# Optimization experiments

Hardware: AMD Instinct MI355X
Metric: run time of the kernel (lower is better)

The kernel has to match this reference:

```python
import jax, jax.numpy as jnp
import numpy as np

N_NODES = 131072
N_EDGES = 8388608
NUM_GRAPHS = 1024
GAMMA = 1.0


def setup_inputs() -> dict:
    key = jax.random.key(0)
    k1, k2, k3 = jax.random.split(key, 3)
    node_pos = jax.random.normal(k1, (N_NODES, 2), dtype=jnp.float32)
    full_edge_index = jax.random.randint(k2, (2, N_EDGES), 0, N_NODES, dtype=jnp.int64)
    batch_idx = jnp.sort(jax.random.randint(k3, (N_NODES,), 0, NUM_GRAPHS, dtype=jnp.int64))
    return {"node_pos": node_pos, "full_edge_index": full_edge_index, "batch_idx": batch_idx}


def reference(node_pos, full_edge_index, batch_idx):
    # gather edge endpoints: [E, 2] each
    start = node_pos[full_edge_index[0]]
    end = node_pos[full_edge_index[1]]
    # Euclidean length per edge, then exponential distance decay
    eu = jnp.linalg.norm(end - start, axis=1)          # [E]
    edge_occlusion = jnp.exp(-GAMMA * eu)              # [E]
    # scatter-sum per graph, keyed by graph id of the source node
    index = batch_idx[full_edge_index[0]]              # [E]
    graph_occlusion = jax.ops.segment_sum(edge_occlusion, index, num_segments=NUM_GRAPHS)
    # reduce = torch.mean over graphs
    return jnp.mean(graph_occlusion)
```

## Files before the change

### kernel.cpp

```cpp
#include <hip/hip_runtime.h>


#define N_EDGES_C   8388608
#define GRID1       2048
#define BLOCK1      256
#define TOTAL_THR   (GRID1 * BLOCK1)
#define N_GROUPS    (N_EDGES_C / 4)
#define GROUPS_PER_THREAD (N_GROUPS / TOTAL_THR)
#define INV_NUM_GRAPHS (1.0f / 1024.0f)

typedef int v4i __attribute__((ext_vector_type(4)));

__global__ __launch_bounds__(BLOCK1) void occlusion_partial(
    const float2* __restrict__ pos,
    const v4i*    __restrict__ src4,
    const v4i*    __restrict__ dst4,
    float*        __restrict__ partials)
{
    const int tid = blockIdx.x * blockDim.x + threadIdx.x;

    v4i s[GROUPS_PER_THREAD], d[GROUPS_PER_THREAD];
    #pragma unroll
    for (int j = 0; j < GROUPS_PER_THREAD; ++j) {
        s[j] = __builtin_nontemporal_load(&src4[tid + j * TOTAL_THR]);
        d[j] = __builtin_nontemporal_load(&dst4[tid + j * TOTAL_THR]);
    }

    float2 ps[16], pd[16];
    #pragma unroll
    for (int j = 0; j < GROUPS_PER_THREAD; ++j) {
        #pragma unroll
        for (int k = 0; k < 4; ++k) {
            ps[j * 4 + k] = pos[s[j][k]];
            pd[j * 4 + k] = pos[d[j][k]];
        }
    }

    float acc0 = 0.f, acc1 = 0.f, acc2 = 0.f, acc3 = 0.f;
    #pragma unroll
    for (int k = 0; k < 4; ++k) {
        float dx, dy;
        dx = pd[k +  0].x - ps[k +  0].x;  dy = pd[k +  0].y - ps[k +  0].y;
        acc0 += __expf(-sqrtf(dx * dx + dy * dy));
        dx = pd[k +  4].x - ps[k +  4].x;  dy = pd[k +  4].y - ps[k +  4].y;
        acc1 += __expf(-sqrtf(dx * dx + dy * dy));
        dx = pd[k +  8].x - ps[k +  8].x;  dy = pd[k +  8].y - ps[k +  8].y;
        acc2 += __expf(-sqrtf(dx * dx + dy * dy));
        dx = pd[k + 12].x - ps[k + 12].x;  dy = pd[k + 12].y - ps[k + 12].y;
        acc3 += __expf(-sqrtf(dx * dx + dy * dy));
    }
    float acc = (acc0 + acc1) + (acc2 + acc3);

    #pragma unroll
    for (int off = 32; off > 0; off >>= 1)
        acc += __shfl_down(acc, off, 64);

    __shared__ float wave_sums[BLOCK1 / 64];
    const int lane = threadIdx.x & 63;
    const int wid  = threadIdx.x >> 6;
    if (lane == 0) wave_sums[wid] = acc;
    __syncthreads();

    if (threadIdx.x == 0) {
        partials[blockIdx.x] = (wave_sums[0] + wave_sums[1]) +
                               (wave_sums[2] + wave_sums[3]);
    }
}

__global__ __launch_bounds__(256) void occlusion_final(
    const float* __restrict__ partials,
    float*       __restrict__ out)
{
    float a = 0.f;
    #pragma unroll
    for (int i = 0; i < GRID1 / 256; ++i)
        a += partials[threadIdx.x + i * 256];

    #pragma unroll
    for (int off = 32; off > 0; off >>= 1)
        a += __shfl_down(a, off, 64);

    __shared__ float w[4];
    if ((threadIdx.x & 63) == 0) w[threadIdx.x >> 6] = a;
    __syncthreads();
    if (threadIdx.x == 0)
        out[0] = ((w[0] + w[1]) + (w[2] + w[3])) * INV_NUM_GRAPHS;
}

extern "C" void kernel_launch(void* const* d_in, const int* in_sizes, int n_in,
                              void* d_out, int out_size, void* d_ws, size_t ws_size,
                              hipStream_t stream) {
    const float* node_pos = (const float*)d_in[0];
    const int*   edge_idx = (const int*)d_in[1];

    const int E = in_sizes[1] / 2;
    const int* src = edge_idx;
    const int* dst = edge_idx + E;

    float* partials = (float*)d_ws;
    float* out = (float*)d_out;

    occlusion_partial<<<GRID1, BLOCK1, 0, stream>>>(
        reinterpret_cast<const float2*>(node_pos),
        reinterpret_cast<const v4i*>(src),
        reinterpret_cast<const v4i*>(dst),
        partials);
    occlusion_final<<<1, 256, 0, stream>>>(partials, out);
}
```

Before: 166.8 us.

## Stage first quarter of node positions as half2 in LDS per block

Each 1024-thread block first copies the first 32768 node positions into shared memory, converted to half2, then loops over its edge groups. Endpoints with index below that bound are read from LDS and the rest from global memory. The grid shrinks to 256 blocks of 1024 threads and the final reduce changes to match. The aim is to replace about a quarter of the random global gathers with LDS reads. In exchange every block re-reads and converts the table, the 128KB of LDS limits occupancy, and positions lose precision to fp16.

Measured after the change: 166.5 us. Within noise of the previous version (-0.2%).

```diff
diff --git a/kernel.cpp b/kernel.cpp
--- a/kernel.cpp
+++ b/kernel.cpp
@@ -1,12 +1,14 @@
 #include <hip/hip_runtime.h>
+#include <hip/hip_fp16.h>
 
 
 #define N_EDGES_C   8388608
-#define GRID1       2048
-#define BLOCK1      256
+#define STAGED      32768
+#define BLOCK1      1024
+#define GRID1       256
 #define TOTAL_THR   (GRID1 * BLOCK1)
 #define N_GROUPS    (N_EDGES_C / 4)
-#define GROUPS_PER_THREAD (N_GROUPS / TOTAL_THR)
+#define GPT         (N_GROUPS / TOTAL_THR)
 #define INV_NUM_GRAPHS (1.0f / 1024.0f)
 
 typedef int v4i __attribute__((ext_vector_type(4)));
@@ -17,36 +19,55 @@
     const v4i*    __restrict__ dst4,
     float*        __restrict__ partials)
 {
-    const int tid = blockIdx.x * blockDim.x + threadIdx.x;
+    __shared__ __half2 tab[STAGED];
 
-    v4i s[GROUPS_PER_THREAD], d[GROUPS_PER_THREAD];
-    #pragma unroll
-    for (int j = 0; j < GROUPS_PER_THREAD; ++j) {
-        s[j] = __builtin_nontemporal_load(&src4[tid + j * TOTAL_THR]);
-        d[j] = __builtin_nontemporal_load(&dst4[tid + j * TOTAL_THR]);
-    }
-
-    float2 ps[16], pd[16];
-    #pragma unroll
-    for (int j = 0; j < GROUPS_PER_THREAD; ++j) {
+    {
+        const float4* p4 = reinterpret_cast<const float4*>(pos);
         #pragma unroll
-        for (int k = 0; k < 4; ++k) {
-            ps[j * 4 + k] = pos[s[j][k]];
-            pd[j * 4 + k] = pos[d[j][k]];
+        for (int i = threadIdx.x; i < STAGED / 2; i += BLOCK1) {
+            float4 v = p4[i];
+            tab[2 * i + 0] = __floats2half2_rn(v.x, v.y);
+            tab[2 * i + 1] = __floats2half2_rn(v.z, v.w);
         }
     }
+    __syncthreads();
+
+    const int tid = blockIdx.x * BLOCK1 + threadIdx.x;
 
     float acc0 = 0.f, acc1 = 0.f, acc2 = 0.f, acc3 = 0.f;
     #pragma unroll
-    for (int k = 0; k < 4; ++k) {
+    for (int j = 0; j < GPT; ++j) {
+        const int g = tid + j * TOTAL_THR;
+        const v4i s = __builtin_nontemporal_load(&src4[g]);
+        const v4i d = __builtin_nontemporal_load(&dst4[g]);
+
+        float2 ps[4], pd[4];
+        #pragma unroll
+        for (int k = 0; k < 4; ++k) {
+            const int is = s[k];
+            const int id = d[k];
+            if (is < STAGED) {
+                __half2 h = tab[is];
+                ps[k] = make_float2(__low2float(h), __high2float(h));
+            } else {
+                ps[k] = pos[is];
+            }
+            if (id < STAGED) {
+                __half2 h = tab[id];
+                pd[k] = make_float2(__low2float(h), __high2float(h));
+            } else {
+                pd[k] = pos[id];
+            }
+        }
+
         float dx, dy;
-        dx = pd[k +  0].x - ps[k +  0].x;  dy = pd[k +  0].y - ps[k +  0].y;
+        dx = pd[0].x - ps[0].x;  dy = pd[0].y - ps[0].y;
         acc0 += __expf(-sqrtf(dx * dx + dy * dy));
-        dx = pd[k +  4].x - ps[k +  4].x;  dy = pd[k +  4].y - ps[k +  4].y;
+        dx = pd[1].x - ps[1].x;  dy = pd[1].y - ps[1].y;
         acc1 += __expf(-sqrtf(dx * dx + dy * dy));
-        dx = pd[k +  8].x - ps[k +  8].x;  dy = pd[k +  8].y - ps[k +  8].y;
+        dx = pd[2].x - ps[2].x;  dy = pd[2].y - ps[2].y;
         acc2 += __expf(-sqrtf(dx * dx + dy * dy));
-        dx = pd[k + 12].x - ps[k + 12].x;  dy = pd[k + 12].y - ps[k + 12].y;
+        dx = pd[3].x - ps[3].x;  dy = pd[3].y - ps[3].y;
         acc3 += __expf(-sqrtf(dx * dx + dy * dy));
     }
     float acc = (acc0 + acc1) + (acc2 + acc3);
@@ -55,15 +76,18 @@
     for (int off = 32; off > 0; off >>= 1)
         acc += __shfl_down(acc, off, 64);
 
-    __shared__ float wave_sums[BLOCK1 / 64];
+    __syncthreads();
+    float* ws = reinterpret_cast<float*>(tab);
     const int lane = threadIdx.x & 63;
     const int wid  = threadIdx.x >> 6;
-    if (lane == 0) wave_sums[wid] = acc;
+    if (lane == 0) ws[wid] = acc;
     __syncthreads();
 
     if (threadIdx.x == 0) {
-        partials[blockIdx.x] = (wave_sums[0] + wave_sums[1]) +
-                               (wave_sums[2] + wave_sums[3]);
+        float s = 0.f;
+        #pragma unroll
+        for (int w = 0; w < BLOCK1 / 64; ++w) s += ws[w];
+        partials[blockIdx.x] = s;
     }
 }
 
@@ -71,10 +95,7 @@
     const float* __restrict__ partials,
     float*       __restrict__ out)
 {
-    float a = 0.f;
-    #pragma unroll
-    for (int i = 0; i < GRID1 / 256; ++i)
-        a += partials[threadIdx.x + i * 256];
+    float a = partials[threadIdx.x];
 
     #pragma unroll
     for (int off = 32; off > 0; off >>= 1)
```
